# Optimization experiments

Measured on AMD Instinct MI355X. Metric: run time of the kernel, lower is better.

## Reference

```python
import jax, jax.numpy as jnp
import numpy as np

B, S, D, F, E = 4, 2048, 1024, 4096, 8


def setup_inputs() -> dict:
    key = jax.random.key(0)
    ks = jax.random.split(key, 7)
    s1 = 1.0 / np.sqrt(D)
    s2 = 1.0 / np.sqrt(F)
    x = jax.random.normal(ks[0], (B, S, D), dtype=jnp.float32)
    # Stacked expert weights: linear1 (D->F), linear2 (F->D), torch default uniform init
    W1 = jax.random.uniform(ks[1], (E, D, F), jnp.float32, -s1, s1)
    b1 = jax.random.uniform(ks[2], (E, F), jnp.float32, -s1, s1)
    W2 = jax.random.uniform(ks[3], (E, F, D), jnp.float32, -s2, s2)
    b2 = jax.random.uniform(ks[4], (E, D), jnp.float32, -s2, s2)
    Wr = jax.random.uniform(ks[5], (D, E), jnp.float32, -s1, s1)
    br = jax.random.uniform(ks[6], (E,), jnp.float32, -s1, s1)
    return {"x": x, "W1": W1, "b1": b1, "W2": W2, "b2": b2, "Wr": Wr, "br": br}


def reference(x, W1, b1, W2, b2, Wr, br):
    b, s, d = x.shape
    e = Wr.shape[1]
    logits = x @ Wr + br                      # [B,S,E]
    idx = jnp.argmax(logits, axis=-1)         # top-1 expert per token
    probs = jax.nn.softmax(logits, axis=-1)
    gates = jnp.take_along_axis(probs, idx[..., None], axis=-1)[..., 0]  # [B,S]
    xf = x.reshape(-1, d)                     # [N,D]
    idxf = idx.reshape(-1)
    gf = gates.reshape(-1)
    out = jnp.zeros_like(xf)
    for ei in range(e):                       # fixed small expert count
        h = jax.nn.gelu(xf @ W1[ei] + b1[ei], approximate=False)  # exact gelu like F.gelu
        y = h @ W2[ei] + b2[ei]
        mask = (idxf == ei).astype(xf.dtype)
        out = out + y * (gf * mask)[:, None]
    return out.reshape(b, s, d)
```

## Files before the change

### kernel.cpp

```cpp
#include <hip/hip_runtime.h>
#include <stdint.h>
#include <math.h>

#define NTOK 8192
#define DIM  1024
#define FDIM 4096
#define NEXP 8

typedef __bf16 bf16x8 __attribute__((ext_vector_type(8)));
typedef float floatx4 __attribute__((ext_vector_type(4)));
typedef unsigned int u32;

__device__ __forceinline__ unsigned short f2b(float f) {
  union { float f; unsigned u; } v; v.f = f;
  return (unsigned short)((v.u + 0x7fffu + ((v.u >> 16) & 1u)) >> 16);
}

__device__ __forceinline__ float gelu_f(float x) {
  float u = 1.5957691216f * x * (1.0f + 0.044715f * x * x);
  return x / (1.0f + __expf(-u));
}

__device__ __forceinline__ void async_cp16(const unsigned short* g, unsigned short* l) {
  __builtin_amdgcn_global_load_lds((__attribute__((address_space(1))) u32*)g,
                                   (__attribute__((address_space(3))) u32*)l, 16, 0, 0);
}

__global__ __launch_bounds__(256) void router_k(
    const float* __restrict__ x, const float* __restrict__ Wr,
    const float* __restrict__ br, int* __restrict__ idx,
    float* __restrict__ gate, int* __restrict__ ctrl) {
  int t = (int)((blockIdx.x * 256 + threadIdx.x) >> 6);
  int lane = threadIdx.x & 63;
  const float* xr = x + (size_t)t * DIM;
  float acc[NEXP];
#pragma unroll
  for (int e = 0; e < NEXP; e++) acc[e] = 0.f;
#pragma unroll
  for (int k = 0; k < DIM / 64; k++) {
    int d = k * 64 + lane;
    float xv = xr[d];
    const float4* wp = (const float4*)(Wr + (size_t)d * NEXP);
    float4 w0 = wp[0], w1 = wp[1];
    acc[0] += xv * w0.x; acc[1] += xv * w0.y;
    acc[2] += xv * w0.z; acc[3] += xv * w0.w;
    acc[4] += xv * w1.x; acc[5] += xv * w1.y;
    acc[6] += xv * w1.z; acc[7] += xv * w1.w;
  }
#pragma unroll
  for (int off = 32; off > 0; off >>= 1) {
#pragma unroll
    for (int e = 0; e < NEXP; e++) acc[e] += __shfl_xor(acc[e], off, 64);
  }
  if (lane == 0) {
    float mx = -3.4e38f; int best = 0;
#pragma unroll
    for (int e = 0; e < NEXP; e++) {
      float l = acc[e] + br[e];
      if (l > mx) { mx = l; best = e; }
    }
    float s = 0.f;
#pragma unroll
    for (int e = 0; e < NEXP; e++) s += expf(acc[e] + br[e] - mx);
    idx[t] = best;
    gate[t] = 1.f / s;
    atomicAdd(&ctrl[best], 1);
  }
}

__global__ void scan_k(int* __restrict__ ctrl) {
  int off = 0, ts = 0;
  ctrl[8] = 0; ctrl[25] = 0;
  for (int e = 0; e < NEXP; e++) {
    off += ctrl[e];                 ctrl[9 + e]  = off;
    ts  += (ctrl[e] + 127) >> 7;    ctrl[26 + e] = ts;
  }
}

__global__ __launch_bounds__(256) void scatter_k(
    const float* __restrict__ x, const int* __restrict__ idx,
    const float* __restrict__ gate, int* __restrict__ ctrl,
    unsigned short* __restrict__ Xb, int* __restrict__ token_dst,
    float* __restrict__ gate_p) {
  __shared__ int s_pos;
  int t = blockIdx.x;
  if (threadIdx.x == 0) {
    int e = idx[t];
    s_pos = ctrl[8 + e] + atomicAdd(&ctrl[17 + e], 1);
  }
  __syncthreads();
  int pos = s_pos;
  if (threadIdx.x == 0) { token_dst[pos] = t; gate_p[pos] = gate[t]; }
  float4 v = ((const float4*)(x + (size_t)t * DIM))[threadIdx.x];
  ushort4 o;
  o.x = f2b(v.x); o.y = f2b(v.y); o.z = f2b(v.z); o.w = f2b(v.w);
  ((ushort4*)(Xb + (size_t)pos * DIM))[threadIdx.x] = o;
}

__global__ __launch_bounds__(256) void transpose_cvt2_k(
    const float* __restrict__ W1, unsigned short* __restrict__ W1b,
    const float* __restrict__ W2, unsigned short* __restrict__ W2b) {
  __shared__ float tile[64][65];
  __shared__ unsigned short obuf[64][72];
  int z = blockIdx.z;
  const float* in; unsigned short* out; int R, C, tc, tr;
  if (z < NEXP) {
    in = W1 + (size_t)z * DIM * FDIM; out = W1b + (size_t)z * DIM * FDIM;
    R = DIM; C = FDIM; tc = blockIdx.x; tr = blockIdx.y;
  } else {
    int e = z - NEXP;
    in = W2 + (size_t)e * FDIM * DIM; out = W2b + (size_t)e * FDIM * DIM;
    R = FDIM; C = DIM; tc = blockIdx.y; tr = blockIdx.x;
  }
  int c0 = tc * 64, r0 = tr * 64;
  int t = threadIdx.x;
  int rr = t >> 4, cc = (t & 15) * 4;
#pragma unroll
  for (int k = 0; k < 64; k += 16) {
    float4 v = *(const float4*)&in[(size_t)(r0 + rr + k) * C + c0 + cc];
    tile[rr + k][cc] = v.x; tile[rr + k][cc + 1] = v.y;
    tile[rr + k][cc + 2] = v.z; tile[rr + k][cc + 3] = v.w;
  }
  __syncthreads();
  int cr = t >> 4, rb = (t & 15) * 4;
#pragma unroll
  for (int k = 0; k < 64; k += 16) {
    ushort4 o;
    o.x = f2b(tile[rb + 0][cr + k]); o.y = f2b(tile[rb + 1][cr + k]);
    o.z = f2b(tile[rb + 2][cr + k]); o.w = f2b(tile[rb + 3][cr + k]);
    *(ushort4*)&obuf[cr + k][rb] = o;
  }
  __syncthreads();
  int r2 = t >> 3, c8 = (t & 7) * 8;
#pragma unroll
  for (int k = 0; k < 64; k += 32)
    *(uint4*)&out[(size_t)(c0 + r2 + k) * R + r0 + c8] = *(const uint4*)&obuf[r2 + k][c8];
}

__global__ __launch_bounds__(256) void gemm1_k(
    const unsigned short* __restrict__ Amat, const unsigned short* __restrict__ Bmat,
    const float* __restrict__ bias, unsigned short* __restrict__ Hout,
    const int* __restrict__ ctrl) {
  __shared__ unsigned short lds[17408];
  unsigned short* A_lds = lds;
  unsigned short* B_lds = lds + 8192;

  int mt = blockIdx.y;
  if (mt >= ctrl[33]) return;
  int e = 0;
  while (e < 7 && ctrl[26 + e] <= mt) e++;
  int mt_local = mt - ctrl[25 + e];
  int m0 = ctrl[8 + e] + mt_local * 128;
  int cnt = ctrl[e] - mt_local * 128; if (cnt > 128) cnt = 128;
  int c0 = blockIdx.x * 128;
  const unsigned short* B = Bmat + (size_t)e * FDIM * DIM;

  int tid = threadIdx.x;
  int lane = tid & 63, wave = tid >> 6;
  int wr = wave >> 1, wc = wave & 1;
  int grp = lane >> 4, m16 = lane & 15;

  int lr = lane >> 3;
  int cchunk = (lane & 7) ^ lr;
  const unsigned short* srcA[4];
  const unsigned short* srcB[4];
  unsigned short* dstA[4];
  unsigned short* dstB[4];
#pragma unroll
  for (int q = 0; q < 4; q++) {
    int brow = wave * 32 + q * 8;
    int arow = m0 + brow + lr; if (arow > NTOK - 1) arow = NTOK - 1;
    srcA[q] = Amat + (size_t)arow * DIM + cchunk * 8;
    srcB[q] = B + (size_t)(c0 + brow + lr) * DIM + cchunk * 8;
    dstA[q] = A_lds + brow * 64;
    dstB[q] = B_lds + brow * 64;
  }

  floatx4 acc[4][4];
  floatx4 zero = {0.f, 0.f, 0.f, 0.f};
#pragma unroll
  for (int i = 0; i < 4; i++)
#pragma unroll
    for (int j = 0; j < 4; j++) acc[i][j] = zero;

  int x7 = m16 & 7;
  int rowA[4], rowB[4];
#pragma unroll
  for (int i = 0; i < 4; i++) {
    rowA[i] = (wr * 64 + i * 16 + m16) * 64;
    rowB[i] = (wc * 64 + i * 16 + m16) * 64;
  }

  for (int kk = 0; kk < DIM; kk += 64) {
#pragma unroll
    for (int q = 0; q < 4; q++) async_cp16(srcA[q], dstA[q]);
#pragma unroll
    for (int q = 0; q < 4; q++) async_cp16(srcB[q], dstB[q]);
#pragma unroll
    for (int q = 0; q < 4; q++) { srcA[q] += 64; srcB[q] += 64; }
    __syncthreads();
    bf16x8 af[2][4], bfr[2][4];
#pragma unroll
    for (int h = 0; h < 2; h++) {
      int off = (((h << 2) | grp) ^ x7) << 3;
#pragma unroll
      for (int i = 0; i < 4; i++) {
        af[h][i]  = *(const bf16x8*)&A_lds[rowA[i] + off];
        bfr[h][i] = *(const bf16x8*)&B_lds[rowB[i] + off];
      }
    }
#pragma unroll
    for (int h = 0; h < 2; h++)
#pragma unroll
      for (int i = 0; i < 4; i++)
#pragma unroll
        for (int j = 0; j < 4; j++)
          acc[i][j] = __builtin_amdgcn_mfma_f32_16x16x32_bf16(af[h][i], bfr[h][j], acc[i][j], 0, 0, 0);
    __syncthreads();
  }

  float bs[4];
#pragma unroll
  for (int j = 0; j < 4; j++) bs[j] = bias[(size_t)e * FDIM + c0 + wc * 64 + j * 16 + m16];

  unsigned short* st = lds + wave * 4352;
#pragma unroll
  for (int i = 0; i < 4; i++)
#pragma unroll
    for (int j = 0; j < 4; j++)
#pragma unroll
      for (int r = 0; r < 4; r++)
        st[(i * 16 + grp * 4 + r) * 68 + j * 16 + m16] = f2b(gelu_f(acc[i][j][r] + bs[j]));
  __syncthreads();
  int lr8 = lane >> 3, c8 = (lane & 7) * 8;
  int colb = c0 + wc * 64 + c8;
#pragma unroll
  for (int rr = 0; rr < 8; rr++) {
    int row = rr * 8 + lr8;
    int gm = wr * 64 + row;
    if (gm < cnt) {
      uint2 a = *(const uint2*)&st[row * 68 + c8];
      uint2 b = *(const uint2*)&st[row * 68 + c8 + 4];
      uint4 v; v.x = a.x; v.y = a.y; v.z = b.x; v.w = b.y;
      *(uint4*)&Hout[(size_t)(m0 + gm) * FDIM + colb] = v;
    }
  }
}

__global__ __launch_bounds__(256) void gemm2_k(
    const unsigned short* __restrict__ Hmat, const unsigned short* __restrict__ W2b,
    const float* __restrict__ b2, float* __restrict__ out,
    const int* __restrict__ token_dst, const float* __restrict__ gate_p,
    const int* __restrict__ ctrl) {
  __shared__ unsigned short lds[16384];
  unsigned short* A_lds = lds;
  unsigned short* B_lds = lds + 8192;

  int mt = blockIdx.y;
  if (mt >= ctrl[33]) return;
  int e = 0;
  while (e < 7 && ctrl[26 + e] <= mt) e++;
  int mt_local = mt - ctrl[25 + e];
  int m0 = ctrl[8 + e] + mt_local * 128;
  int cnt = ctrl[e] - mt_local * 128; if (cnt > 128) cnt = 128;
  int c0 = blockIdx.x * 128;
  const unsigned short* B = W2b + (size_t)e * DIM * FDIM;

  int tid = threadIdx.x;
  int lane = tid & 63, wave = tid >> 6;
  int wr = wave >> 1, wc = wave & 1;
  int grp = lane >> 4, m16 = lane & 15;

  int lr = lane >> 3;
  int cchunk = (lane & 7) ^ lr;
  const unsigned short* srcA[4];
  const unsigned short* srcB[4];
  unsigned short* dstA[4];
  unsigned short* dstB[4];
#pragma unroll
  for (int q = 0; q < 4; q++) {
    int brow = wave * 32 + q * 8;
    int arow = m0 + brow + lr; if (arow > NTOK - 1) arow = NTOK - 1;
    srcA[q] = Hmat + (size_t)arow * FDIM + cchunk * 8;
    srcB[q] = B + (size_t)(c0 + brow + lr) * FDIM + cchunk * 8;
    dstA[q] = A_lds + brow * 64;
    dstB[q] = B_lds + brow * 64;
  }

  floatx4 acc[4][4];
  floatx4 zero = {0.f, 0.f, 0.f, 0.f};
#pragma unroll
  for (int i = 0; i < 4; i++)
#pragma unroll
    for (int j = 0; j < 4; j++) acc[i][j] = zero;

  int x7 = m16 & 7;
  int rowA[4], rowB[4];
#pragma unroll
  for (int i = 0; i < 4; i++) {
    rowA[i] = (wr * 64 + i * 16 + m16) * 64;
    rowB[i] = (wc * 64 + i * 16 + m16) * 64;
  }

  for (int kk = 0; kk < FDIM; kk += 64) {
#pragma unroll
    for (int q = 0; q < 4; q++) async_cp16(srcA[q], dstA[q]);
#pragma unroll
    for (int q = 0; q < 4; q++) async_cp16(srcB[q], dstB[q]);
#pragma unroll
    for (int q = 0; q < 4; q++) { srcA[q] += 64; srcB[q] += 64; }
    __syncthreads();
    bf16x8 af[2][4], bfr[2][4];
#pragma unroll
    for (int h = 0; h < 2; h++) {
      int off = (((h << 2) | grp) ^ x7) << 3;
#pragma unroll
      for (int i = 0; i < 4; i++) {
        af[h][i]  = *(const bf16x8*)&A_lds[rowA[i] + off];
        bfr[h][i] = *(const bf16x8*)&B_lds[rowB[i] + off];
      }
    }
#pragma unroll
    for (int h = 0; h < 2; h++)
#pragma unroll
      for (int i = 0; i < 4; i++)
#pragma unroll
        for (int j = 0; j < 4; j++)
          acc[i][j] = __builtin_amdgcn_mfma_f32_16x16x32_bf16(af[h][i], bfr[h][j], acc[i][j], 0, 0, 0);
    __syncthreads();
  }

  float bs[4];
#pragma unroll
  for (int j = 0; j < 4; j++) bs[j] = b2[(size_t)e * DIM + c0 + wc * 64 + j * 16 + m16];

#pragma unroll
  for (int i = 0; i < 4; i++) {
    int rb = wr * 64 + i * 16 + grp * 4;
#pragma unroll
    for (int r = 0; r < 4; r++) {
      int lm = rb + r;
      if (lm < cnt) {
        int t = token_dst[m0 + lm];
        float g = gate_p[m0 + lm];
#pragma unroll
        for (int j = 0; j < 4; j++) {
          int col = c0 + wc * 64 + j * 16 + m16;
          out[(size_t)t * DIM + col] = (acc[i][j][r] + bs[j]) * g;
        }
      }
    }
  }
}

extern "C" void kernel_launch(void* const* d_in, const int* in_sizes, int n_in,
                              void* d_out, int out_size, void* d_ws, size_t ws_size,
                              hipStream_t stream) {
  const float* x  = (const float*)d_in[0];
  const float* W1 = (const float*)d_in[1];
  const float* b1 = (const float*)d_in[2];
  const float* W2 = (const float*)d_in[3];
  const float* b2 = (const float*)d_in[4];
  const float* Wr = (const float*)d_in[5];
  const float* br = (const float*)d_in[6];
  float* out = (float*)d_out;

  char* w = (char*)d_ws;
  int*   ctrl      = (int*)w;
  int*   idx       = (int*)(w + 1024);
  float* gate      = (float*)(w + 1024 + 4 * NTOK);
  int*   token_dst = (int*)(w + 1024 + 8 * NTOK);
  float* gate_p    = (float*)(w + 1024 + 12 * NTOK);
  unsigned short* Xb  = (unsigned short*)(w + (1ull << 18));
  unsigned short* H   = (unsigned short*)(w + (20ull << 20));
  unsigned short* W1b = (unsigned short*)(w + (88ull << 20));
  unsigned short* W2b = (unsigned short*)(w + (156ull << 20));

  hipMemsetAsync(ctrl, 0, 256, stream);
  router_k<<<NTOK / 4, 256, 0, stream>>>(x, Wr, br, idx, gate, ctrl);
  scan_k<<<1, 1, 0, stream>>>(ctrl);
  scatter_k<<<NTOK, 256, 0, stream>>>(x, idx, gate, ctrl, Xb, token_dst, gate_p);
  transpose_cvt2_k<<<dim3(64, 16, 16), 256, 0, stream>>>(W1, W1b, W2, W2b);
  gemm1_k<<<dim3(FDIM / 128, 72), 256, 0, stream>>>(Xb, W1b, b1, H, ctrl);
  gemm2_k<<<dim3(DIM / 128, 72), 256, 0, stream>>>(H, W2b, b2, out, token_dst, gate_p, ctrl);
}
```

Before: 807.5 us.

## Split-K gemm2 with atomic accumulation and fold scan kernel into consumers

The second expert GEMM is split along K into two halves via a z grid dimension. Partial results are accumulated into a zeroed output with float atomicAdd, and only the first half adds the bias. This doubles the block count of the under-occupied gemm2 grid at the cost of an output memset and atomic traffic. Separately, the single-thread scan kernel is removed, and expert offsets and tile counts are recomputed inline from the counts in scatter and in both GEMMs, saving one launch.

```diff
diff --git a/kernel.cpp b/kernel.cpp
--- a/kernel.cpp
+++ b/kernel.cpp
@@ -24,6 +24,25 @@
 __device__ __forceinline__ void async_cp16(const unsigned short* g, unsigned short* l) {
   __builtin_amdgcn_global_load_lds((__attribute__((address_space(1))) u32*)g,
                                    (__attribute__((address_space(3))) u32*)l, 16, 0, 0);
+}
+
+__device__ __forceinline__ void expert_tile(const int* __restrict__ ctrl, int mt,
+                                            int& e, int& m0, int& cnt, int& ntiles) {
+  int off = 0, ts = 0;
+  e = 0; m0 = 0; cnt = 0;
+#pragma unroll
+  for (int i = 0; i < NEXP; i++) {
+    int c = ctrl[i];
+    int nt = (c + 127) >> 7;
+    if (mt >= ts && mt < ts + nt) {
+      e = i;
+      m0 = off + (mt - ts) * 128;
+      cnt = c - (mt - ts) * 128;
+    }
+    ts += nt; off += c;
+  }
+  ntiles = ts;
+  if (cnt > 128) cnt = 128;
 }
 
 __global__ __launch_bounds__(256) void router_k(
@@ -68,15 +87,6 @@
   }
 }
 
-__global__ void scan_k(int* __restrict__ ctrl) {
-  int off = 0, ts = 0;
-  ctrl[8] = 0; ctrl[25] = 0;
-  for (int e = 0; e < NEXP; e++) {
-    off += ctrl[e];                 ctrl[9 + e]  = off;
-    ts  += (ctrl[e] + 127) >> 7;    ctrl[26 + e] = ts;
-  }
-}
-
 __global__ __launch_bounds__(256) void scatter_k(
     const float* __restrict__ x, const int* __restrict__ idx,
     const float* __restrict__ gate, int* __restrict__ ctrl,
@@ -86,7 +96,10 @@
   int t = blockIdx.x;
   if (threadIdx.x == 0) {
     int e = idx[t];
-    s_pos = ctrl[8 + e] + atomicAdd(&ctrl[17 + e], 1);
+    int off = 0;
+#pragma unroll
+    for (int i = 0; i < NEXP; i++) off += (i < e) ? ctrl[i] : 0;
+    s_pos = off + atomicAdd(&ctrl[17 + e], 1);
   }
   __syncthreads();
   int pos = s_pos;
@@ -146,12 +159,9 @@
   unsigned short* B_lds = lds + 8192;
 
   int mt = blockIdx.y;
-  if (mt >= ctrl[33]) return;
-  int e = 0;
-  while (e < 7 && ctrl[26 + e] <= mt) e++;
-  int mt_local = mt - ctrl[25 + e];
-  int m0 = ctrl[8 + e] + mt_local * 128;
-  int cnt = ctrl[e] - mt_local * 128; if (cnt > 128) cnt = 128;
+  int e, m0, cnt, ntiles;
+  expert_tile(ctrl, mt, e, m0, cnt, ntiles);
+  if (mt >= ntiles) return;
   int c0 = blockIdx.x * 128;
   const unsigned short* B = Bmat + (size_t)e * FDIM * DIM;
 
@@ -257,14 +267,13 @@
   unsigned short* B_lds = lds + 8192;
 
   int mt = blockIdx.y;
-  if (mt >= ctrl[33]) return;
-  int e = 0;
-  while (e < 7 && ctrl[26 + e] <= mt) e++;
-  int mt_local = mt - ctrl[25 + e];
-  int m0 = ctrl[8 + e] + mt_local * 128;
-  int cnt = ctrl[e] - mt_local * 128; if (cnt > 128) cnt = 128;
+  int e, m0, cnt, ntiles;
+  expert_tile(ctrl, mt, e, m0, cnt, ntiles);
+  if (mt >= ntiles) return;
   int c0 = blockIdx.x * 128;
-  const unsigned short* B = W2b + (size_t)e * DIM * FDIM;
+  int k0 = blockIdx.z * (FDIM / 2);
+  const unsigned short* B = W2b + (size_t)e * DIM * FDIM + k0;
+  const unsigned short* A = Hmat + k0;
 
   int tid = threadIdx.x;
   int lane = tid & 63, wave = tid >> 6;
@@ -281,7 +290,7 @@
   for (int q = 0; q < 4; q++) {
     int brow = wave * 32 + q * 8;
     int arow = m0 + brow + lr; if (arow > NTOK - 1) arow = NTOK - 1;
-    srcA[q] = Hmat + (size_t)arow * FDIM + cchunk * 8;
+    srcA[q] = A + (size_t)arow * FDIM + cchunk * 8;
     srcB[q] = B + (size_t)(c0 + brow + lr) * FDIM + cchunk * 8;
     dstA[q] = A_lds + brow * 64;
     dstB[q] = B_lds + brow * 64;
@@ -302,7 +311,7 @@
     rowB[i] = (wc * 64 + i * 16 + m16) * 64;
   }
 
-  for (int kk = 0; kk < FDIM; kk += 64) {
+  for (int kk = 0; kk < FDIM / 2; kk += 64) {
 #pragma unroll
     for (int q = 0; q < 4; q++) async_cp16(srcA[q], dstA[q]);
 #pragma unroll
@@ -332,7 +341,8 @@
 
   float bs[4];
 #pragma unroll
-  for (int j = 0; j < 4; j++) bs[j] = b2[(size_t)e * DIM + c0 + wc * 64 + j * 16 + m16];
+  for (int j = 0; j < 4; j++)
+    bs[j] = (blockIdx.z == 0) ? b2[(size_t)e * DIM + c0 + wc * 64 + j * 16 + m16] : 0.f;
 
 #pragma unroll
   for (int i = 0; i < 4; i++) {
@@ -346,7 +356,7 @@
 #pragma unroll
         for (int j = 0; j < 4; j++) {
           int col = c0 + wc * 64 + j * 16 + m16;
-          out[(size_t)t * DIM + col] = (acc[i][j][r] + bs[j]) * g;
+          atomicAdd(&out[(size_t)t * DIM + col], (acc[i][j][r] + bs[j]) * g);
         }
       }
     }
@@ -377,10 +387,10 @@
   unsigned short* W2b = (unsigned short*)(w + (156ull << 20));
 
   hipMemsetAsync(ctrl, 0, 256, stream);
+  hipMemsetAsync(out, 0, (size_t)NTOK * DIM * 4, stream);
   router_k<<<NTOK / 4, 256, 0, stream>>>(x, Wr, br, idx, gate, ctrl);
-  scan_k<<<1, 1, 0, stream>>>(ctrl);
   scatter_k<<<NTOK, 256, 0, stream>>>(x, idx, gate, ctrl, Xb, token_dst, gate_p);
   transpose_cvt2_k<<<dim3(64, 16, 16), 256, 0, stream>>>(W1, W1b, W2, W2b);
   gemm1_k<<<dim3(FDIM / 128, 72), 256, 0, stream>>>(Xb, W1b, b1, H, ctrl);
-  gemm2_k<<<dim3(DIM / 128, 72), 256, 0, stream>>>(H, W2b, b2, out, token_dst, gate_p, ctrl);
-}
+  gemm2_k<<<dim3(DIM / 128, 72, 2), 256, 0, stream>>>(H, W2b, b2, out, token_dst, gate_p, ctrl);
+}
```

New measurement: 821.1 us. About the same (+1.7%).
